# Kernel optimization log

Hardware: AMD Instinct MI355X
Metric: run time of the kernel (lower is better)

## Reference

```python
import jax, jax.numpy as jnp
import numpy as np

B, D, H = 64, 512, 8
EPS = 1e-8


def setup_inputs() -> dict:
    key = jax.random.key(0)
    k1, k2, k3 = jax.random.split(key, 3)
    x = jax.random.normal(k1, (B, D), dtype=jnp.float32)
    # alphas/betas: one scalar per (head, transform); columns = (query, key, value)
    alphas = jax.random.uniform(k2, (H, 3), dtype=jnp.float32)
    betas = jax.random.uniform(k3, (H, 3), dtype=jnp.float32)
    return {"x": x, "alphas": alphas, "betas": betas}


def reference(x, alphas, betas):
    # x: [B, D]; alphas, betas: [H, 3] (query, key, value scalar affine params per head)
    d = x.shape[-1]
    # qkv[h, t, b, d] = alphas[h, t] * x[b, d] + betas[h, t]  (ones vector -> plain bias)
    qkv = alphas[:, :, None, None] * x[None, None, :, :] + betas[:, :, None, None]  # [H,3,B,D]
    q, k, v = qkv[:, 0], qkv[:, 1], qkv[:, 2]  # each [H, B, D]
    # diff[h,b,i,j] = |q[h,b,j] - k[h,b,i]|  (row i = key feature, col j = query feature)
    diff = jnp.abs(q[:, :, None, :] - k[:, :, :, None]) + EPS  # [H, B, D, D]
    sim = jax.nn.softmax(1.0 / diff, axis=-1) / jnp.sqrt(jnp.float32(d))
    # attended[h,b,i] = sum_j sim[h,b,i,j] * v[h,b,j]  (batched matvec)
    attended = jnp.einsum("hbij,hbj->hbi", sim, v)  # [H, B, D]
    return x + attended.sum(axis=0)
```

## Files before the change

### kernel.cpp

```cpp
#include <hip/hip_runtime.h>
#include <math.h>

#define BB 64
#define DD 512
#define HH 8
#define EPS 1e-8f

__device__ float g_xsorted[BB][DD];
__device__ int   g_perm[BB][DD];

__device__ __forceinline__ float fast_rcp(float d) {
    return __builtin_amdgcn_rcpf(d);
}

__global__ __launch_bounds__(DD) void sort_kernel(const float* __restrict__ x,
                                                  float* __restrict__ out)
{
    const int b   = blockIdx.x;
    const int tid = threadIdx.x;
    __shared__ float sv[DD];
    const float xi = x[b * DD + tid];
    sv[tid] = xi;
    out[b * DD + tid] = 0.0f;
    __syncthreads();

    int cnt = 0;
    #pragma unroll 4
    for (int j = 0; j < DD; j += 4) {
        float4 v = *(const float4*)&sv[j];
        cnt += (int)((v.x < xi) | ((v.x == xi) & ((j + 0) < tid)));
        cnt += (int)((v.y < xi) | ((v.y == xi) & ((j + 1) < tid)));
        cnt += (int)((v.z < xi) | ((v.z == xi) & ((j + 2) < tid)));
        cnt += (int)((v.w < xi) | ((v.w == xi) & ((j + 3) < tid)));
    }
    g_xsorted[b][cnt] = xi;
    g_perm[b][cnt]    = tid;
}

__global__ __launch_bounds__(512, 8) void flattn_kernel(
    const float* __restrict__ x,
    const float* __restrict__ alphas,
    const float* __restrict__ betas,
    float* __restrict__ out)
{
    const int b  = blockIdx.x;
    const int ic = blockIdx.y;
    const int h  = blockIdx.z;

    __shared__ float xs[DD];
    __shared__ float xss[DD];
    __shared__ float mind_sh[2][256];
    __shared__ float ss_sh[256];
    __shared__ float sx_sh[256];

    const int tid  = threadIdx.x;
    const int ii   = tid & 255;
    const int jc   = tid >> 8;
    const int rank = ic * 256 + ii;

    const float a0 = alphas[h * 3 + 0];
    const float a1 = alphas[h * 3 + 1];
    const float a2 = alphas[h * 3 + 2];
    const float b0 = betas[h * 3 + 0];
    const float b1 = betas[h * 3 + 1];
    const float b2 = betas[h * 3 + 2];

    xs[tid]  = x[b * DD + tid];
    xss[tid] = g_xsorted[b][tid];
    __syncthreads();

    const float xi = xss[rank];
    const float c  = b0 - fmaf(a1, xi, b1);

    const float ra0 = fast_rcp(a0);
    const float u   = -c * ra0;

    int pos = 0;
    #pragma unroll
    for (int s = 512; s > 0; s >>= 1) {
        int p = pos + s;
        float v = xss[(p <= 512 ? p : 512) - 1];
        pos = (p <= 512 && v < u) ? p : pos;
    }
    float mind_hat = 3.0e38f;
    #pragma unroll
    for (int q = -2; q <= 1; ++q) {
        int cidx = pos + q;
        if (cidx >= 0 && cidx < DD)
            mind_hat = fminf(mind_hat, fabsf(fmaf(a0, xss[cidx], c)));
    }
    const float mhat = fast_rcp(mind_hat + EPS);

    const float th  = fast_rcp(fmaxf(mhat - 30.0f, 1e-30f));
    const float tha = fmaf(th * 1.0001f, ra0, 1e-6f);
    const float xlo = u - tha;
    const float xhi = u + tha;

    int lo = 0, hi = 0;
    #pragma unroll
    for (int s = 512; s > 0; s >>= 1) {
        int pl = lo + s, ph = hi + s;
        float vl = xss[(pl <= 512 ? pl : 512) - 1];
        float vh = xss[(ph <= 512 ? ph : 512) - 1];
        lo = (pl <= 512 && vl <  xlo) ? pl : lo;
        hi = (ph <= 512 && vh <= xhi) ? ph : hi;
    }
    lo = max(lo - 2, 0);
    hi = min(hi + 2, DD);
    const int len = hi - lo;

    const bool lane_peaked = (a0 > 1e-6f) && (mhat > 45.0f) && (len <= 128);
    const bool peaked = __all(lane_peaked);

    const float log2e = 1.4426950408889634f;

    float md = 3.0e38f;
    int wl = 0, wh = 0;
    const int j0 = jc * 256;
    if (peaked) {
        const int mid = lo + ((len + 1) >> 1);
        wl = jc ? mid : lo;
        wh = jc ? hi  : mid;
        for (int k = wl; k < wh; ++k)
            md = fminf(md, fabsf(fmaf(a0, xss[k], c)));
    } else {
        #pragma unroll 4
        for (int j = j0; j < j0 + 256; j += 4) {
            float4 x4 = *(const float4*)&xs[j];
            md = fminf(md, fabsf(fmaf(a0, x4.x, c)));
            md = fminf(md, fabsf(fmaf(a0, x4.y, c)));
            md = fminf(md, fabsf(fmaf(a0, x4.z, c)));
            md = fminf(md, fabsf(fmaf(a0, x4.w, c)));
        }
    }
    mind_sh[jc][ii] = md;
    __syncthreads();

    const float mind  = fminf(mind_sh[0][ii], mind_sh[1][ii]);
    const float m     = fast_rcp(mind + EPS);
    const float negml = -m * log2e;

    float ss = 0.0f, sx = 0.0f;
    if (peaked) {
        for (int k = wl; k < wh; ++k) {
            float xv = xss[k];
            float t  = fmaf(a0, xv, c);
            float r  = fast_rcp(fabsf(t) + EPS);
            float s  = __builtin_amdgcn_exp2f(fmaf(r, log2e, negml));
            ss += s; sx = fmaf(s, xv, sx);
        }
    } else {
        #pragma unroll 2
        for (int j = j0; j < j0 + 256; j += 4) {
            float4 x4 = *(const float4*)&xs[j];
            {
                float t = fmaf(a0, x4.x, c);
                float r = fast_rcp(fabsf(t) + EPS);
                float s = __builtin_amdgcn_exp2f(fmaf(r, log2e, negml));
                ss += s; sx = fmaf(s, x4.x, sx);
            }
            {
                float t = fmaf(a0, x4.y, c);
                float r = fast_rcp(fabsf(t) + EPS);
                float s = __builtin_amdgcn_exp2f(fmaf(r, log2e, negml));
                ss += s; sx = fmaf(s, x4.y, sx);
            }
            {
                float t = fmaf(a0, x4.z, c);
                float r = fast_rcp(fabsf(t) + EPS);
                float s = __builtin_amdgcn_exp2f(fmaf(r, log2e, negml));
                ss += s; sx = fmaf(s, x4.z, sx);
            }
            {
                float t = fmaf(a0, x4.w, c);
                float r = fast_rcp(fabsf(t) + EPS);
                float s = __builtin_amdgcn_exp2f(fmaf(r, log2e, negml));
                ss += s; sx = fmaf(s, x4.w, sx);
            }
        }
    }

    if (jc == 1) { ss_sh[ii] = ss; sx_sh[ii] = sx; }
    __syncthreads();
    if (jc == 0) {
        ss += ss_sh[ii];
        sx += sx_sh[ii];
        const float scale = 0.04419417382415922f;
        float sv  = fmaf(a2, sx, b2 * ss);
        float att = sv * fast_rcp(ss) * scale;
        if (h == 0) att += xi;
        const int i_orig = g_perm[b][rank];
        atomicAdd(&out[b * DD + i_orig], att);
    }
}

extern "C" void kernel_launch(void* const* d_in, const int* in_sizes, int n_in,
                              void* d_out, int out_size, void* d_ws, size_t ws_size,
                              hipStream_t stream) {
    const float* x      = (const float*)d_in[0];
    const float* alphas = (const float*)d_in[1];
    const float* betas  = (const float*)d_in[2];
    float* out = (float*)d_out;

    sort_kernel<<<dim3(BB), dim3(DD), 0, stream>>>(x, out);

    dim3 grid(BB, 2, HH);
    dim3 block(512);
    flattn_kernel<<<grid, block, 0, stream>>>(x, alphas, betas, out);
}
```

Baseline: 102.7 us.

## Use wave-uniform window bounds with vectorized loads and drop exact min pass

Replaces the per-lane peaked test with a wave-wide union window built from shuffle min/max of lo and hi. When the union spans at most 256 sorted entries, the kernel skips the exact minimum-distance pass, uses the binary-search estimate mind_hat as the softmax max, and evaluates only the window with float4 loads split between the two half-blocks. This removes the divergent per-lane loops and the extra min-reduction sweep. In exchange, the window test no longer checks peakedness thresholds, and correctness relies on mind_hat being the true minimum and on the truncation bound.

Measured after the change: 105.2 us. 2.4% more time.

```diff
diff --git a/kernel.cpp b/kernel.cpp
--- a/kernel.cpp
+++ b/kernel.cpp
@@ -72,58 +72,58 @@
     const float xi = xss[rank];
     const float c  = b0 - fmaf(a1, xi, b1);
 
-    const float ra0 = fast_rcp(a0);
-    const float u   = -c * ra0;
-
-    int pos = 0;
+    int lo = 0, hi = DD;
+    float mind_hat = 3.0e38f;
+    if (a0 > 1e-6f) {
+        const float ra0 = fast_rcp(a0);
+        const float u   = -c * ra0;
+
+        int pos = 0;
+        #pragma unroll
+        for (int s = 512; s > 0; s >>= 1) {
+            int p = pos + s;
+            float v = xss[(p <= 512 ? p : 512) - 1];
+            pos = (p <= 512 && v < u) ? p : pos;
+        }
+        #pragma unroll
+        for (int q = -2; q <= 1; ++q) {
+            int ci = pos + q;
+            if (ci >= 0 && ci < DD)
+                mind_hat = fminf(mind_hat, fabsf(fmaf(a0, xss[ci], c)));
+        }
+        const float mhat = fast_rcp(mind_hat + EPS);
+
+        const float th  = fast_rcp(fmaxf(mhat - 30.0f, 1e-30f));
+        const float tha = fmaf(th * 1.0001f, ra0, 1e-6f);
+        const float xlo = u - tha;
+        const float xhi = u + tha;
+
+        int l = 0, hc = 0;
+        #pragma unroll
+        for (int s = 512; s > 0; s >>= 1) {
+            int pl = l + s, ph = hc + s;
+            float vl = xss[(pl <= 512 ? pl : 512) - 1];
+            float vh = xss[(ph <= 512 ? ph : 512) - 1];
+            l  = (pl <= 512 && vl <  xlo) ? pl : l;
+            hc = (ph <= 512 && vh <= xhi) ? ph : hc;
+        }
+        lo = max(l - 2, 0);
+        hi = min(hc + 2, DD);
+    }
+
+    int ulo = lo, uhi = hi;
     #pragma unroll
-    for (int s = 512; s > 0; s >>= 1) {
-        int p = pos + s;
-        float v = xss[(p <= 512 ? p : 512) - 1];
-        pos = (p <= 512 && v < u) ? p : pos;
-    }
-    float mind_hat = 3.0e38f;
-    #pragma unroll
-    for (int q = -2; q <= 1; ++q) {
-        int cidx = pos + q;
-        if (cidx >= 0 && cidx < DD)
-            mind_hat = fminf(mind_hat, fabsf(fmaf(a0, xss[cidx], c)));
-    }
-    const float mhat = fast_rcp(mind_hat + EPS);
-
-    const float th  = fast_rcp(fmaxf(mhat - 30.0f, 1e-30f));
-    const float tha = fmaf(th * 1.0001f, ra0, 1e-6f);
-    const float xlo = u - tha;
-    const float xhi = u + tha;
-
-    int lo = 0, hi = 0;
-    #pragma unroll
-    for (int s = 512; s > 0; s >>= 1) {
-        int pl = lo + s, ph = hi + s;
-        float vl = xss[(pl <= 512 ? pl : 512) - 1];
-        float vh = xss[(ph <= 512 ? ph : 512) - 1];
-        lo = (pl <= 512 && vl <  xlo) ? pl : lo;
-        hi = (ph <= 512 && vh <= xhi) ? ph : hi;
-    }
-    lo = max(lo - 2, 0);
-    hi = min(hi + 2, DD);
-    const int len = hi - lo;
-
-    const bool lane_peaked = (a0 > 1e-6f) && (mhat > 45.0f) && (len <= 128);
-    const bool peaked = __all(lane_peaked);
+    for (int msk = 1; msk < 64; msk <<= 1) {
+        ulo = min(ulo, __shfl_xor(ulo, msk, 64));
+        uhi = max(uhi, __shfl_xor(uhi, msk, 64));
+    }
+    const bool windowed = (uhi - ulo) <= 256;
 
     const float log2e = 1.4426950408889634f;
-
-    float md = 3.0e38f;
-    int wl = 0, wh = 0;
     const int j0 = jc * 256;
-    if (peaked) {
-        const int mid = lo + ((len + 1) >> 1);
-        wl = jc ? mid : lo;
-        wh = jc ? hi  : mid;
-        for (int k = wl; k < wh; ++k)
-            md = fminf(md, fabsf(fmaf(a0, xss[k], c)));
-    } else {
+
+    if (!windowed) {
+        float md = 3.0e38f;
         #pragma unroll 4
         for (int j = j0; j < j0 + 256; j += 4) {
             float4 x4 = *(const float4*)&xs[j];
@@ -132,22 +132,52 @@
             md = fminf(md, fabsf(fmaf(a0, x4.z, c)));
             md = fminf(md, fabsf(fmaf(a0, x4.w, c)));
         }
-    }
-    mind_sh[jc][ii] = md;
-    __syncthreads();
-
-    const float mind  = fminf(mind_sh[0][ii], mind_sh[1][ii]);
-    const float m     = fast_rcp(mind + EPS);
-    const float negml = -m * log2e;
+        mind_sh[jc][ii] = md;
+    }
+    __syncthreads();
+
+    float m_;
+    if (windowed) {
+        m_ = fast_rcp(mind_hat + EPS);
+    } else {
+        m_ = fast_rcp(fminf(mind_sh[0][ii], mind_sh[1][ii]) + EPS);
+    }
+    const float negml = -m_ * log2e;
 
     float ss = 0.0f, sx = 0.0f;
-    if (peaked) {
-        for (int k = wl; k < wh; ++k) {
-            float xv = xss[k];
-            float t  = fmaf(a0, xv, c);
-            float r  = fast_rcp(fabsf(t) + EPS);
-            float s  = __builtin_amdgcn_exp2f(fmaf(r, log2e, negml));
-            ss += s; sx = fmaf(s, xv, sx);
+    if (windowed) {
+        const int base = ulo & ~3;
+        const int e4   = min((uhi + 3) & ~3, DD);
+        const int nb   = (e4 - base) >> 2;
+        const int nbh  = (nb + 1) >> 1;
+        const int kb0  = base + ((jc == 0) ? 0 : nbh * 4);
+        const int kend = base + ((jc == 0) ? nbh * 4 : nb * 4);
+        for (int k = kb0; k < kend; k += 4) {
+            float4 x4 = *(const float4*)&xss[k];
+            {
+                float t = fmaf(a0, x4.x, c);
+                float r = fast_rcp(fabsf(t) + EPS);
+                float s = __builtin_amdgcn_exp2f(fmaf(r, log2e, negml));
+                ss += s; sx = fmaf(s, x4.x, sx);
+            }
+            {
+                float t = fmaf(a0, x4.y, c);
+                float r = fast_rcp(fabsf(t) + EPS);
+                float s = __builtin_amdgcn_exp2f(fmaf(r, log2e, negml));
+                ss += s; sx = fmaf(s, x4.y, sx);
+            }
+            {
+                float t = fmaf(a0, x4.z, c);
+                float r = fast_rcp(fabsf(t) + EPS);
+                float s = __builtin_amdgcn_exp2f(fmaf(r, log2e, negml));
+                ss += s; sx = fmaf(s, x4.z, sx);
+            }
+            {
+                float t = fmaf(a0, x4.w, c);
+                float r = fast_rcp(fabsf(t) + EPS);
+                float s = __builtin_amdgcn_exp2f(fmaf(r, log2e, negml));
+                ss += s; sx = fmaf(s, x4.w, sx);
+            }
         }
     } else {
         #pragma unroll 2
```

## Compact peaked rows into per-wave queues to cut divergence in softmax windows

Applied to the files above, without the earlier changes.

Only the first half of the block now locates each row's window. Rows are sorted into a shared queue, narrow-window rows at the front and wide rows at the back, so a whole wave usually takes the same path instead of falling back to the dense loop when any lane is wide. The exact minimum-distance pass is dropped: the estimate taken near the binary-search position is used directly as the softmax max, and log2 scaling is folded into the reciprocal. The window threshold is also tightened (cap 64, drop margin 16), which risks accuracy if the estimated max or the truncated window miss significant terms.

Result: no change. 102.7 us (-0.1%).

```diff
diff --git a/kernel.cpp b/kernel.cpp
--- a/kernel.cpp
+++ b/kernel.cpp
@@ -5,6 +5,8 @@
 #define DD 512
 #define HH 8
 #define EPS 1e-8f
+#define CAP 64
+#define TDROP 16.0f
 
 __device__ float g_xsorted[BB][DD];
 __device__ int   g_perm[BB][DD];
@@ -49,14 +51,17 @@
 
     __shared__ float xs[DD];
     __shared__ float xss[DD];
-    __shared__ float mind_sh[2][256];
     __shared__ float ss_sh[256];
     __shared__ float sx_sh[256];
-
-    const int tid  = threadIdx.x;
-    const int ii   = tid & 255;
-    const int jc   = tid >> 8;
-    const int rank = ic * 256 + ii;
+    __shared__ float c_sh[256];
+    __shared__ float ml_sh[256];
+    __shared__ int   lohi_sh[256];
+    __shared__ int   q_sh[256];
+    __shared__ int   cnt_sh[2];
+
+    const int tid = threadIdx.x;
+    const int ii  = tid & 255;
+    const int jc  = tid >> 8;
 
     const float a0 = alphas[h * 3 + 0];
     const float a1 = alphas[h * 3 + 1];
@@ -67,114 +72,124 @@
 
     xs[tid]  = x[b * DD + tid];
     xss[tid] = g_xsorted[b][tid];
-    __syncthreads();
-
-    const float xi = xss[rank];
-    const float c  = b0 - fmaf(a1, xi, b1);
-
-    const float ra0 = fast_rcp(a0);
-    const float u   = -c * ra0;
-
-    int pos = 0;
-    #pragma unroll
-    for (int s = 512; s > 0; s >>= 1) {
-        int p = pos + s;
-        float v = xss[(p <= 512 ? p : 512) - 1];
-        pos = (p <= 512 && v < u) ? p : pos;
-    }
-    float mind_hat = 3.0e38f;
-    #pragma unroll
-    for (int q = -2; q <= 1; ++q) {
-        int cidx = pos + q;
-        if (cidx >= 0 && cidx < DD)
-            mind_hat = fminf(mind_hat, fabsf(fmaf(a0, xss[cidx], c)));
-    }
-    const float mhat = fast_rcp(mind_hat + EPS);
-
-    const float th  = fast_rcp(fmaxf(mhat - 30.0f, 1e-30f));
-    const float tha = fmaf(th * 1.0001f, ra0, 1e-6f);
-    const float xlo = u - tha;
-    const float xhi = u + tha;
-
-    int lo = 0, hi = 0;
-    #pragma unroll
-    for (int s = 512; s > 0; s >>= 1) {
-        int pl = lo + s, ph = hi + s;
-        float vl = xss[(pl <= 512 ? pl : 512) - 1];
-        float vh = xss[(ph <= 512 ? ph : 512) - 1];
-        lo = (pl <= 512 && vl <  xlo) ? pl : lo;
-        hi = (ph <= 512 && vh <= xhi) ? ph : hi;
-    }
-    lo = max(lo - 2, 0);
-    hi = min(hi + 2, DD);
-    const int len = hi - lo;
-
-    const bool lane_peaked = (a0 > 1e-6f) && (mhat > 45.0f) && (len <= 128);
-    const bool peaked = __all(lane_peaked);
-
-    const float log2e = 1.4426950408889634f;
-
-    float md = 3.0e38f;
-    int wl = 0, wh = 0;
-    const int j0 = jc * 256;
-    if (peaked) {
-        const int mid = lo + ((len + 1) >> 1);
-        wl = jc ? mid : lo;
-        wh = jc ? hi  : mid;
-        for (int k = wl; k < wh; ++k)
-            md = fminf(md, fabsf(fmaf(a0, xss[k], c)));
-    } else {
-        #pragma unroll 4
-        for (int j = j0; j < j0 + 256; j += 4) {
-            float4 x4 = *(const float4*)&xs[j];
-            md = fminf(md, fabsf(fmaf(a0, x4.x, c)));
-            md = fminf(md, fabsf(fmaf(a0, x4.y, c)));
-            md = fminf(md, fabsf(fmaf(a0, x4.z, c)));
-            md = fminf(md, fabsf(fmaf(a0, x4.w, c)));
-        }
-    }
-    mind_sh[jc][ii] = md;
-    __syncthreads();
-
-    const float mind  = fminf(mind_sh[0][ii], mind_sh[1][ii]);
-    const float m     = fast_rcp(mind + EPS);
-    const float negml = -m * log2e;
+    if (tid < 2) cnt_sh[tid] = 0;
+    __syncthreads();
+
+    const float LN2    = 0.6931471805599453f;
+    const float EPSLN2 = 6.931471805599453e-9f;
+
+    if (jc == 0) {
+        const int rank = ic * 256 + ii;
+        const float xi = xss[rank];
+        const float c  = b0 - fmaf(a1, xi, b1);
+
+        const float ra0 = fast_rcp(a0);
+        float u = -c * ra0;
+        if (!(u == u)) u = 0.0f;
+
+        int pos = 0;
+        #pragma unroll
+        for (int s = 512; s > 0; s >>= 1) {
+            int p = pos + s;
+            float v = xss[(p <= 512 ? p : 512) - 1];
+            pos = (p <= 512 && v < u) ? p : pos;
+        }
+        float mind_hat = 3.0e38f;
+        #pragma unroll
+        for (int q = -2; q <= 1; ++q) {
+            int ci = pos + q;
+            if (ci >= 0 && ci < DD)
+                mind_hat = fminf(mind_hat, fabsf(fmaf(a0, xss[ci], c)));
+        }
+        const float ml    = fast_rcp(fmaf(mind_hat, LN2, EPSLN2));
+        const float m_nat = fast_rcp(mind_hat + EPS);
+
+        const float th  = fast_rcp(fmaxf(m_nat - TDROP, 1e-30f));
+        const float tha = fmaf(th * 1.001f, ra0, 1e-6f);
+        const float xlo = u - tha;
+        const float xhi = u + tha;
+
+        int l = 0, hc = 0;
+        #pragma unroll
+        for (int s = 512; s > 0; s >>= 1) {
+            int pl = l + s, ph = hc + s;
+            float vl = xss[(pl <= 512 ? pl : 512) - 1];
+            float vh = xss[(ph <= 512 ? ph : 512) - 1];
+            l  = (pl <= 512 && vl <  xlo) ? pl : l;
+            hc = (ph <= 512 && vh <= xhi) ? ph : hc;
+        }
+        const int lo = max(l - 2, 0);
+        const int hi = min(hc + 2, DD);
+
+        c_sh[ii]    = c;
+        ml_sh[ii]   = ml;
+        lohi_sh[ii] = lo | (hi << 16);
+        if (hi - lo <= CAP) {
+            int p = atomicAdd(&cnt_sh[0], 1);
+            q_sh[p] = ii;
+        } else {
+            int p = atomicAdd(&cnt_sh[1], 1);
+            q_sh[255 - p] = ii;
+        }
+    }
+    __syncthreads();
+
+    const int   nP    = cnt_sh[0];
+    const int   e     = q_sh[ii];
+    const int   meta  = lohi_sh[e];
+    const int   elo   = meta & 0xffff;
+    const int   ehi   = meta >> 16;
+    const float ce    = c_sh[e];
+    const float mle   = ml_sh[e];
+    const bool  isflat = (ii >= nP);
 
     float ss = 0.0f, sx = 0.0f;
-    if (peaked) {
-        for (int k = wl; k < wh; ++k) {
-            float xv = xss[k];
-            float t  = fmaf(a0, xv, c);
-            float r  = fast_rcp(fabsf(t) + EPS);
-            float s  = __builtin_amdgcn_exp2f(fmaf(r, log2e, negml));
-            ss += s; sx = fmaf(s, xv, sx);
-        }
-    } else {
+
+    {
+        const int mylen = isflat ? 0 : (ehi - elo);
+        const int half1 = (mylen + 1) >> 1;
+        const int wl    = elo + (jc ? half1 : 0);
+        const int wn    = jc ? (mylen - half1) : half1;
+        int T = wn;
+        #pragma unroll
+        for (int msk = 1; msk < 64; msk <<= 1)
+            T = max(T, __shfl_xor(T, msk, 64));
+        for (int k = 0; k < T; ++k) {
+            const bool  valid = (k < wn);
+            const float xv = xss[min(wl + k, DD - 1)];
+            const float t  = fmaf(a0, xv, ce);
+            const float w  = fmaf(fabsf(t), LN2, EPSLN2);
+            float s = __builtin_amdgcn_exp2f(fast_rcp(w) - mle);
+            s = valid ? s : 0.0f;
+            ss += s;
+            sx = fmaf(s, xv, sx);
+        }
+    }
+
+    if (__any(isflat)) {
+        const float mlf = isflat ? mle : __builtin_inff();
+        const int j0 = jc * 256;
         #pragma unroll 2
         for (int j = j0; j < j0 + 256; j += 4) {
             float4 x4 = *(const float4*)&xs[j];
             {
-                float t = fmaf(a0, x4.x, c);
-                float r = fast_rcp(fabsf(t) + EPS);
-                float s = __builtin_amdgcn_exp2f(fmaf(r, log2e, negml));
+                float t = fmaf(a0, x4.x, ce);
+                float s = __builtin_amdgcn_exp2f(fast_rcp(fmaf(fabsf(t), LN2, EPSLN2)) - mlf);
                 ss += s; sx = fmaf(s, x4.x, sx);
             }
             {
-                float t = fmaf(a0, x4.y, c);
-                float r = fast_rcp(fabsf(t) + EPS);
-                float s = __builtin_amdgcn_exp2f(fmaf(r, log2e, negml));
+                float t = fmaf(a0, x4.y, ce);
+                float s = __builtin_amdgcn_exp2f(fast_rcp(fmaf(fabsf(t), LN2, EPSLN2)) - mlf);
                 ss += s; sx = fmaf(s, x4.y, sx);
             }
             {
-                float t = fmaf(a0, x4.z, c);
-                float r = fast_rcp(fabsf(t) + EPS);
-                float s = __builtin_amdgcn_exp2f(fmaf(r, log2e, negml));
+                float t = fmaf(a0, x4.z, ce);
+                float s = __builtin_amdgcn_exp2f(fast_rcp(fmaf(fabsf(t), LN2, EPSLN2)) - mlf);
                 ss += s; sx = fmaf(s, x4.z, sx);
             }
             {
-                float t = fmaf(a0, x4.w, c);
-                float r = fast_rcp(fabsf(t) + EPS);
-                float s = __builtin_amdgcn_exp2f(fmaf(r, log2e, negml));
+                float t = fmaf(a0, x4.w, ce);
+                float s = __builtin_amdgcn_exp2f(fast_rcp(fmaf(fabsf(t), LN2, EPSLN2)) - mlf);
                 ss += s; sx = fmaf(s, x4.w, sx);
             }
         }
@@ -188,9 +203,9 @@
         const float scale = 0.04419417382415922f;
         float sv  = fmaf(a2, sx, b2 * ss);
         float att = sv * fast_rcp(ss) * scale;
-        if (h == 0) att += xi;
-        const int i_orig = g_perm[b][rank];
-        atomicAdd(&out[b * DD + i_orig], att);
+        const int rank_e = ic * 256 + e;
+        if (h == 0) att += xss[rank_e];
+        atomicAdd(&out[b * DD + g_perm[b][rank_e]], att);
     }
 }
 
```
